# Kernel tuning notes

Hardware: AMD Instinct MI355X
Metric: run time of the kernel (lower is better)

## Reference

```python
import jax, jax.numpy as jnp
import numpy as np

B, S, D = 2, 2048, 1024
H = 16
HD = D // H
SCALE = float(np.sqrt(HD))


def setup_inputs() -> dict:
    key = jax.random.key(0)
    ks = jax.random.split(key, 10)
    def lin(k):
        # xavier_uniform for [out, in] = [D, D]
        bound = float(np.sqrt(6.0 / (D + D)))
        return jax.random.uniform(k, (D, D), jnp.float32, -bound, bound)
    return {
        "hidden_states": jax.random.normal(ks[0], (B, S, D), jnp.float32),
        "attention_mask": jnp.ones((B, S), jnp.float32),
        "Wq": lin(ks[1]), "bq": jnp.zeros((D,), jnp.float32),
        "Wk": lin(ks[2]), "bk": jnp.zeros((D,), jnp.float32),
        "Wv": lin(ks[3]), "bv": jnp.zeros((D,), jnp.float32),
        "Wo": lin(ks[4]), "bo": jnp.zeros((D,), jnp.float32),
    }


def _heads(x):
    # [B,S,D] -> [B,H,S,HD]
    return x.reshape(B, S, H, HD).transpose(0, 2, 1, 3)


def secure_softmax(scores):
    c = jnp.clip(scores, -3.0, 3.0)
    sig = 0.5 + 0.25 * c - 0.01 * c ** 3
    sig = jnp.clip(sig, 0.01, 0.99)
    return sig / (jnp.sum(sig, axis=-1, keepdims=True) + 1e-8)


def reference(hidden_states, attention_mask, Wq, bq, Wk, bk, Wv, bv, Wo, bo):
    q = _heads(hidden_states @ Wq.T + bq)
    k = _heads(hidden_states @ Wk.T + bk)
    v = _heads(hidden_states @ Wv.T + bv)
    # [B,H,S,S]
    scores = jnp.einsum("bhqd,bhkd->bhqk", q, k) / SCALE
    scores = scores + (1.0 - attention_mask[:, None, None, :]) * -10000.0
    probs = secure_softmax(scores)
    ctx = jnp.einsum("bhqk,bhkd->bhqd", probs, v)
    ctx = ctx.transpose(0, 2, 1, 3).reshape(B, S, D)
    return ctx @ Wo.T + bo
```

## Files before the change

### kernel.cpp

```cpp
#include <hip/hip_runtime.h>
#include <stdint.h>

#define B_ 2
#define S_ 2048
#define D_ 1024
#define H_ 16
#define HD_ 64
#define M_ (B_*S_)

typedef __bf16 bf16;
typedef __attribute__((ext_vector_type(8))) __bf16 bf16x8;
typedef __attribute__((ext_vector_type(4))) float f32x4;
typedef __attribute__((ext_vector_type(2))) float f32x2;

__device__ __forceinline__ void gload16(const bf16* g, bf16* l) {
    __builtin_amdgcn_global_load_lds(
        (const __attribute__((address_space(1))) void*)g,
        (__attribute__((address_space(3))) void*)l, 16, 0, 0);
}

__global__ void k_cvt_all(const float* __restrict__ hs,
                          const float* __restrict__ Wq, const float* __restrict__ Wk,
                          const float* __restrict__ Wv, const float* __restrict__ Wo,
                          bf16* __restrict__ hb,
                          bf16* __restrict__ wqb, bf16* __restrict__ wkb,
                          bf16* __restrict__ wvb, bf16* __restrict__ wob) {
    int blk = blockIdx.x;
    const float* s; bf16* d; int base;
    if (blk < 2048) { s = hs; d = hb; base = blk; }
    else {
        int r = blk - 2048; int which = r >> 9; base = r & 511;
        s = (which==0)?Wq:(which==1)?Wk:(which==2)?Wv:Wo;
        d = (which==0)?wqb:(which==1)?wkb:(which==2)?wvb:wob;
    }
    int idx = base*2048 + threadIdx.x*8;
    float4 a = *(const float4*)(s + idx);
    float4 b = *(const float4*)(s + idx + 4);
    bf16 o[8] = {(bf16)a.x,(bf16)a.y,(bf16)a.z,(bf16)a.w,
                 (bf16)b.x,(bf16)b.y,(bf16)b.z,(bf16)b.w};
    *(int4*)(d + idx) = *(const int4*)o;
}

__global__ __launch_bounds__(256) void k_gemm_qkv(
    const bf16* __restrict__ X,
    const bf16* __restrict__ Wq, const bf16* __restrict__ Wk, const bf16* __restrict__ Wv,
    const float* __restrict__ bq, const float* __restrict__ bk, const float* __restrict__ bv,
    bf16* __restrict__ Qo, bf16* __restrict__ Ko, bf16* __restrict__ Vo)
{
    const int z = blockIdx.z;
    const bf16* W = (z==0) ? Wq : (z==1) ? Wk : Wv;
    const float* bias = (z==0) ? bq : (z==1) ? bk : bv;
    const int n0 = blockIdx.x * 128;
    const int m0 = blockIdx.y * 128;
    const int t = threadIdx.x;
    const int w = t >> 6, lane = t & 63, quad = lane >> 4, l15 = lane & 15;
    const int lr = lane >> 3;
    const int lc = (lane & 7) ^ lr;
    const int sx = l15 & 7;
    const int mw = (w >> 1) * 64, nw = (w & 1) * 64;

    __shared__ __align__(16) char smraw[128*136*2];
    bf16* As  = (bf16*)smraw;
    bf16* Bs  = (bf16*)(smraw + 16384);
    bf16* epi = (bf16*)smraw;

    f32x4 acc[4][4];
    #pragma unroll
    for (int i = 0; i < 4; i++)
        #pragma unroll
        for (int j = 0; j < 4; j++)
            acc[i][j] = (f32x4){0.f,0.f,0.f,0.f};

    const bf16* gA = X + (size_t)(m0 + w*8 + lr)*D_ + lc*8;
    const bf16* gB = W + (size_t)(n0 + w*8 + lr)*D_ + lc*8;

    for (int k0 = 0; k0 < D_; k0 += 64) {
        #pragma unroll
        for (int c = 0; c < 4; c++) {
            gload16(gA + (size_t)c*32*D_ + k0, &As[c*2048 + w*512]);
            gload16(gB + (size_t)c*32*D_ + k0, &Bs[c*2048 + w*512]);
        }
        __syncthreads();
        #pragma unroll
        for (int ks = 0; ks < 2; ks++) {
            bf16x8 af[4], bfr[4];
            #pragma unroll
            for (int i = 0; i < 4; i++)
                af[i] = *(const bf16x8*)&As[(mw + i*16 + l15)*64 + (((ks*4+quad)^sx)*8)];
            #pragma unroll
            for (int j = 0; j < 4; j++)
                bfr[j] = *(const bf16x8*)&Bs[(nw + j*16 + l15)*64 + (((ks*4+quad)^sx)*8)];
            #pragma unroll
            for (int i = 0; i < 4; i++)
                #pragma unroll
                for (int j = 0; j < 4; j++)
                    acc[i][j] = __builtin_amdgcn_mfma_f32_16x16x32_bf16(af[i], bfr[j], acc[i][j], 0, 0, 0);
        }
        __syncthreads();
    }

    const float scale = (z == 0) ? 0.125f : 1.0f;
    if (z == 2) {
        #pragma unroll
        for (int j = 0; j < 4; j++) {
            int n = nw + j*16 + l15;
            float bn = bias[n0 + n];
            #pragma unroll
            for (int i = 0; i < 4; i++) {
                int mloc = mw + i*16 + quad*4;
                union { bf16 h4[4]; uint2 u; } pk;
                #pragma unroll
                for (int r = 0; r < 4; r++) pk.h4[r] = (bf16)(acc[i][j][r] + bn);
                *(uint2*)&epi[n*136 + mloc] = pk.u;
            }
        }
    } else {
        #pragma unroll
        for (int j = 0; j < 4; j++) {
            int n = nw + j*16 + l15;
            float bn = bias[n0 + n];
            #pragma unroll
            for (int i = 0; i < 4; i++) {
                int mloc = mw + i*16 + quad*4;
                #pragma unroll
                for (int r = 0; r < 4; r++)
                    epi[(mloc + r)*136 + n] = (bf16)((acc[i][j][r] + bn) * scale);
            }
        }
    }
    __syncthreads();
    if (z == 2) {
        #pragma unroll
        for (int kk = 0; kk < 8; kk++) {
            int c = t + 256*kk;
            int row = c >> 4;
            int mcol = (c & 15) * 8;
            int4 val = *(const int4*)&epi[row*136 + mcol];
            int n = n0 + row; int hh = n >> 6, hd = n & 63;
            int m = m0 + mcol; int bb = m >> 11, s = m & 2047;
            *(int4*)&Vo[((size_t)((bb*H_ + hh)*HD_ + hd))*S_ + s] = val;
        }
    } else {
        bf16* Out = (z == 0) ? Qo : Ko;
        #pragma unroll
        for (int kk = 0; kk < 8; kk++) {
            int c = t + 256*kk;
            int row = c >> 4;
            int ncol = (c & 15) * 8;
            int4 val = *(const int4*)&epi[row*136 + ncol];
            int m = m0 + row; int bb = m >> 11, s = m & 2047;
            int n = n0 + ncol; int hh = n >> 6, hd = n & 63;
            *(int4*)&Out[((size_t)((bb*H_ + hh)*S_ + s))*HD_ + hd] = val;
        }
    }
}

__global__ __launch_bounds__(256) void k_gemm_out(
    const bf16* __restrict__ X, const bf16* __restrict__ W,
    const float* __restrict__ bias, float* __restrict__ Out)
{
    const int n0 = blockIdx.x * 128;
    const int m0 = blockIdx.y * 64;
    const int t = threadIdx.x;
    const int w = t >> 6, lane = t & 63, quad = lane >> 4, l15 = lane & 15;
    const int lr = lane >> 3;
    const int lc = (lane & 7) ^ lr;
    const int sx = l15 & 7;
    const int nw = w * 32;

    __shared__ __align__(16) bf16 As[64*64];
    __shared__ __align__(16) bf16 Bs[128*64];

    f32x4 acc[4][2];
    #pragma unroll
    for (int i = 0; i < 4; i++)
        #pragma unroll
        for (int j = 0; j < 2; j++)
            acc[i][j] = (f32x4){0.f,0.f,0.f,0.f};

    const bf16* gA = X + (size_t)(m0 + w*8 + lr)*D_ + lc*8;
    const bf16* gB = W + (size_t)(n0 + w*8 + lr)*D_ + lc*8;

    for (int k0 = 0; k0 < D_; k0 += 64) {
        #pragma unroll
        for (int c = 0; c < 2; c++)
            gload16(gA + (size_t)c*32*D_ + k0, &As[c*2048 + w*512]);
        #pragma unroll
        for (int c = 0; c < 4; c++)
            gload16(gB + (size_t)c*32*D_ + k0, &Bs[c*2048 + w*512]);
        __syncthreads();
        #pragma unroll
        for (int ks = 0; ks < 2; ks++) {
            bf16x8 af[4], bfr[2];
            #pragma unroll
            for (int i = 0; i < 4; i++)
                af[i] = *(const bf16x8*)&As[(i*16 + l15)*64 + (((ks*4+quad)^sx)*8)];
            #pragma unroll
            for (int j = 0; j < 2; j++)
                bfr[j] = *(const bf16x8*)&Bs[(nw + j*16 + l15)*64 + (((ks*4+quad)^sx)*8)];
            #pragma unroll
            for (int i = 0; i < 4; i++)
                #pragma unroll
                for (int j = 0; j < 2; j++)
                    acc[i][j] = __builtin_amdgcn_mfma_f32_16x16x32_bf16(af[i], bfr[j], acc[i][j], 0, 0, 0);
        }
        __syncthreads();
    }

    #pragma unroll
    for (int j = 0; j < 2; j++) {
        int n = n0 + nw + j*16 + l15;
        float bn = bias[n];
        #pragma unroll
        for (int i = 0; i < 4; i++) {
            int mbase = m0 + i*16 + quad*4;
            #pragma unroll
            for (int r = 0; r < 4; r++)
                Out[(size_t)(mbase + r)*D_ + n] = acc[i][j][r] + bn;
        }
    }
}

__global__ __launch_bounds__(256, 2) void k_attn(
    const bf16* __restrict__ Q, const bf16* __restrict__ K, const bf16* __restrict__ Vt,
    const float* __restrict__ mask, bf16* __restrict__ Ctx)
{
    const int bh = blockIdx.y;
    const int b = bh >> 4, h = bh & 15;
    const int q0 = blockIdx.x * 128;
    const int t = threadIdx.x;
    const int w = t >> 6, lane = t & 63, quad = lane >> 4, l15 = lane & 15;
    const int lr = lane >> 3;
    const int lcV = (lane & 7) ^ lr;
    const int lcK = (lane & 7) ^ ((lr & 3) | ((w & 1) << 2));
    const int sx = l15 & 7;
    const int arow = ((l15 & 12) << 1) | (l15 & 3);

    __shared__ __align__(16) bf16 Ks[2][64*64];
    __shared__ __align__(16) bf16 Vs[2][64*64];

    bf16x8 qf[2][2];
    const bf16* Qbase = Q + ((size_t)bh*S_ + q0 + w*32)*HD_;
    #pragma unroll
    for (int m2 = 0; m2 < 2; m2++)
        #pragma unroll
        for (int ks = 0; ks < 2; ks++)
            qf[m2][ks] = *(const bf16x8*)&Qbase[(size_t)(m2*16 + l15)*HD_ + ks*32 + quad*8];

    f32x4 cacc[2][4];
    #pragma unroll
    for (int i = 0; i < 2; i++)
        #pragma unroll
        for (int j = 0; j < 4; j++)
            cacc[i][j] = (f32x4){0.f,0.f,0.f,0.f};
    f32x2 lacv[2];
    #pragma unroll
    for (int m2 = 0; m2 < 2; m2++) lacv[m2] = (f32x2){0.f,0.f};

    const bf16* KstK = K  + ((size_t)bh*S_  + w*8 + lr)*HD_ + lcK*8;
    const bf16* VstV = Vt + ((size_t)bh*HD_ + w*8 + lr)*S_  + lcV*8;
    const float* mrow = mask + (size_t)b*S_ + quad*8;

    #pragma unroll
    for (int c = 0; c < 2; c++)
        gload16(KstK + (size_t)c*32*HD_, &Ks[0][c*2048 + w*512]);
    #pragma unroll
    for (int c = 0; c < 2; c++)
        gload16(VstV + (size_t)c*32*S_, &Vs[0][c*2048 + w*512]);
    float4 m4[4], m4n[4];
    #pragma unroll
    for (int g = 0; g < 4; g++)
        m4[g] = *(const float4*)&mrow[(g>>1)*32 + (g&1)*4];
    __syncthreads();

    for (int it = 0; it < S_/64; it++) {
        const int cur = it & 1, nxt = cur ^ 1;
        const int k1 = it*64 + 64;
        const bool notlast = (it < S_/64 - 1);

        if (notlast) {
            #pragma unroll
            for (int c = 0; c < 2; c++)
                gload16(KstK + (size_t)(k1 + c*32)*HD_, &Ks[nxt][c*2048 + w*512]);
            #pragma unroll
            for (int c = 0; c < 2; c++)
                gload16(VstV + (size_t)c*32*S_ + k1, &Vs[nxt][c*2048 + w*512]);
            #pragma unroll
            for (int g = 0; g < 4; g++)
                m4n[g] = *(const float4*)&mrow[k1 + (g>>1)*32 + (g&1)*4];
        }

        f32x4 st[4][2];
        #pragma unroll
        for (int g = 0; g < 4; g++) {
            f32x4 sti = (f32x4){m4[g].x, m4[g].y, m4[g].z, m4[g].w} * 10000.f - 10000.f;
            st[g][0] = sti;
            st[g][1] = sti;
        }

        __builtin_amdgcn_s_setprio(1);
        #pragma unroll
        for (int ks = 0; ks < 2; ks++) {
            #pragma unroll
            for (int g = 0; g < 4; g++) {
                const int kk = g >> 1, hf = g & 1;
                bf16x8 af = *(const bf16x8*)&Ks[cur][(arow + hf*4 + kk*32)*64 + (((ks*4+quad)^sx)*8)];
                #pragma unroll
                for (int m2 = 0; m2 < 2; m2++)
                    st[g][m2] = __builtin_amdgcn_mfma_f32_16x16x32_bf16(af, qf[m2][ks], st[g][m2], 0, 0, 0);
            }
        }
        __builtin_amdgcn_s_setprio(0);

        const f32x2 vn3 = {-3.f, -3.f}, vp3 = {3.f, 3.f};
        bf16x8 pa[2][2];
        #pragma unroll
        for (int m2 = 0; m2 < 2; m2++) {
            #pragma unroll
            for (int kk = 0; kk < 2; kk++) {
                union { bf16 h8[8]; bf16x8 v; } pk;
                #pragma unroll
                for (int hf = 0; hf < 2; hf++) {
                    f32x4 sv = st[kk*2 + hf][m2];
                    f32x2 lo = {sv[0], sv[1]};
                    f32x2 hi = {sv[2], sv[3]};
                    lo = __builtin_elementwise_min(__builtin_elementwise_max(lo, vn3), vp3);
                    hi = __builtin_elementwise_min(__builtin_elementwise_max(hi, vn3), vp3);
                    f32x2 tlo = lo * lo * (-0.01f) + 0.25f;
                    f32x2 thi = hi * hi * (-0.01f) + 0.25f;
                    f32x2 slo = lo * tlo + 0.5f;
                    f32x2 shi = hi * thi + 0.5f;
                    lacv[m2] += slo;
                    lacv[m2] += shi;
                    pk.h8[hf*4+0] = (bf16)slo.x; pk.h8[hf*4+1] = (bf16)slo.y;
                    pk.h8[hf*4+2] = (bf16)shi.x; pk.h8[hf*4+3] = (bf16)shi.y;
                }
                pa[m2][kk] = pk.v;
            }
        }

        #pragma unroll
        for (int kk = 0; kk < 2; kk++) {
            bf16x8 vf[4];
            #pragma unroll
            for (int nt = 0; nt < 4; nt++)
                vf[nt] = *(const bf16x8*)&Vs[cur][(nt*16 + l15)*64 + (((kk*4+quad)^sx)*8)];
            __builtin_amdgcn_s_setprio(1);
            #pragma unroll
            for (int m2 = 0; m2 < 2; m2++)
                #pragma unroll
                for (int nt = 0; nt < 4; nt++)
                    cacc[m2][nt] = __builtin_amdgcn_mfma_f32_16x16x32_bf16(pa[m2][kk], vf[nt], cacc[m2][nt], 0, 0, 0);
            __builtin_amdgcn_s_setprio(0);
        }

        __syncthreads();

        #pragma unroll
        for (int g = 0; g < 4; g++) m4[g] = m4n[g];
    }

    float s[2];
    #pragma unroll
    for (int m2 = 0; m2 < 2; m2++) {
        float v = lacv[m2].x + lacv[m2].y;
        v += __shfl_xor(v, 16);
        v += __shfl_xor(v, 32);
        s[m2] = v;
    }

    #pragma unroll
    for (int m2 = 0; m2 < 2; m2++) {
        #pragma unroll
        for (int r = 0; r < 4; r++) {
            float rs = __shfl(s[m2], quad*4 + r);
            float rinv = 1.0f / (rs + 1e-8f);
            size_t row = (size_t)(b*S_ + q0 + w*32 + m2*16 + quad*4 + r);
            #pragma unroll
            for (int nt = 0; nt < 4; nt++)
                Ctx[row*D_ + h*HD_ + nt*16 + l15] = (bf16)(cacc[m2][nt][r] * rinv);
        }
    }
}

extern "C" void kernel_launch(void* const* d_in, const int* in_sizes, int n_in,
                              void* d_out, int out_size, void* d_ws, size_t ws_size,
                              hipStream_t stream) {
    const float* hs   = (const float*)d_in[0];
    const float* mask = (const float*)d_in[1];
    const float* Wq   = (const float*)d_in[2];
    const float* bq   = (const float*)d_in[3];
    const float* Wk   = (const float*)d_in[4];
    const float* bk   = (const float*)d_in[5];
    const float* Wv   = (const float*)d_in[6];
    const float* bv   = (const float*)d_in[7];
    const float* Wo   = (const float*)d_in[8];
    const float* bo   = (const float*)d_in[9];
    float* out = (float*)d_out;

    char* ws = (char*)d_ws;
    const size_t MB = 1024*1024;
    bf16* hb   = (bf16*)(ws);
    bf16* wqb  = (bf16*)(ws + 8*MB);
    bf16* wkb  = (bf16*)(ws + 10*MB);
    bf16* wvb  = (bf16*)(ws + 12*MB);
    bf16* wob  = (bf16*)(ws + 14*MB);
    bf16* qb   = (bf16*)(ws + 16*MB);
    bf16* kb   = (bf16*)(ws + 24*MB);
    bf16* vtb  = (bf16*)(ws + 32*MB);
    bf16* ctxb = (bf16*)(ws + 40*MB);

    k_cvt_all<<<2048 + 4*512, 256, 0, stream>>>(hs, Wq, Wk, Wv, Wo, hb, wqb, wkb, wvb, wob);

    k_gemm_qkv<<<dim3(D_/128, M_/128, 3), 256, 0, stream>>>(
        hb, wqb, wkb, wvb, bq, bk, bv, qb, kb, vtb);

    k_attn<<<dim3(S_/128, B_*H_), 256, 0, stream>>>(qb, kb, vtb, mask, ctxb);

    k_gemm_out<<<dim3(D_/128, M_/64), 256, 0, stream>>>(ctxb, wob, bo, out);
}
```

Baseline: 199.8 us.

## Split attention block work across eight waves of sixteen query rows

```diff
diff --git a/kernel.cpp b/kernel.cpp
--- a/kernel.cpp
+++ b/kernel.cpp
@@ -221,7 +221,7 @@
     }
 }
 
-__global__ __launch_bounds__(256, 2) void k_attn(
+__global__ __launch_bounds__(512, 4) void k_attn(
     const bf16* __restrict__ Q, const bf16* __restrict__ K, const bf16* __restrict__ Vt,
     const float* __restrict__ mask, bf16* __restrict__ Ctx)
 {
@@ -239,34 +239,24 @@
     __shared__ __align__(16) bf16 Ks[2][64*64];
     __shared__ __align__(16) bf16 Vs[2][64*64];
 
-    bf16x8 qf[2][2];
-    const bf16* Qbase = Q + ((size_t)bh*S_ + q0 + w*32)*HD_;
-    #pragma unroll
-    for (int m2 = 0; m2 < 2; m2++)
-        #pragma unroll
-        for (int ks = 0; ks < 2; ks++)
-            qf[m2][ks] = *(const bf16x8*)&Qbase[(size_t)(m2*16 + l15)*HD_ + ks*32 + quad*8];
-
-    f32x4 cacc[2][4];
-    #pragma unroll
-    for (int i = 0; i < 2; i++)
-        #pragma unroll
-        for (int j = 0; j < 4; j++)
-            cacc[i][j] = (f32x4){0.f,0.f,0.f,0.f};
-    f32x2 lacv[2];
-    #pragma unroll
-    for (int m2 = 0; m2 < 2; m2++) lacv[m2] = (f32x2){0.f,0.f};
+    bf16x8 qf[2];
+    const bf16* Qbase = Q + ((size_t)bh*S_ + q0 + w*16)*HD_;
+    #pragma unroll
+    for (int ks = 0; ks < 2; ks++)
+        qf[ks] = *(const bf16x8*)&Qbase[(size_t)l15*HD_ + ks*32 + quad*8];
+
+    f32x4 cacc[4];
+    #pragma unroll
+    for (int j = 0; j < 4; j++)
+        cacc[j] = (f32x4){0.f,0.f,0.f,0.f};
+    f32x2 lacv = (f32x2){0.f,0.f};
 
     const bf16* KstK = K  + ((size_t)bh*S_  + w*8 + lr)*HD_ + lcK*8;
     const bf16* VstV = Vt + ((size_t)bh*HD_ + w*8 + lr)*S_  + lcV*8;
     const float* mrow = mask + (size_t)b*S_ + quad*8;
 
-    #pragma unroll
-    for (int c = 0; c < 2; c++)
-        gload16(KstK + (size_t)c*32*HD_, &Ks[0][c*2048 + w*512]);
-    #pragma unroll
-    for (int c = 0; c < 2; c++)
-        gload16(VstV + (size_t)c*32*S_, &Vs[0][c*2048 + w*512]);
+    gload16(KstK, &Ks[0][w*512]);
+    gload16(VstV, &Vs[0][w*512]);
     float4 m4[4], m4n[4];
     #pragma unroll
     for (int g = 0; g < 4; g++)
@@ -279,24 +269,17 @@
         const bool notlast = (it < S_/64 - 1);
 
         if (notlast) {
-            #pragma unroll
-            for (int c = 0; c < 2; c++)
-                gload16(KstK + (size_t)(k1 + c*32)*HD_, &Ks[nxt][c*2048 + w*512]);
-            #pragma unroll
-            for (int c = 0; c < 2; c++)
-                gload16(VstV + (size_t)c*32*S_ + k1, &Vs[nxt][c*2048 + w*512]);
+            gload16(KstK + (size_t)k1*HD_, &Ks[nxt][w*512]);
+            gload16(VstV + k1,             &Vs[nxt][w*512]);
             #pragma unroll
             for (int g = 0; g < 4; g++)
                 m4n[g] = *(const float4*)&mrow[k1 + (g>>1)*32 + (g&1)*4];
         }
 
-        f32x4 st[4][2];
-        #pragma unroll
-        for (int g = 0; g < 4; g++) {
-            f32x4 sti = (f32x4){m4[g].x, m4[g].y, m4[g].z, m4[g].w} * 10000.f - 10000.f;
-            st[g][0] = sti;
-            st[g][1] = sti;
-        }
+        f32x4 st[4];
+        #pragma unroll
+        for (int g = 0; g < 4; g++)
+            st[g] = (f32x4){m4[g].x, m4[g].y, m4[g].z, m4[g].w} * 10000.f - 10000.f;
 
         __builtin_amdgcn_s_setprio(1);
         #pragma unroll
@@ -305,38 +288,33 @@
             for (int g = 0; g < 4; g++) {
                 const int kk = g >> 1, hf = g & 1;
                 bf16x8 af = *(const bf16x8*)&Ks[cur][(arow + hf*4 + kk*32)*64 + (((ks*4+quad)^sx)*8)];
-                #pragma unroll
-                for (int m2 = 0; m2 < 2; m2++)
-                    st[g][m2] = __builtin_amdgcn_mfma_f32_16x16x32_bf16(af, qf[m2][ks], st[g][m2], 0, 0, 0);
+                st[g] = __builtin_amdgcn_mfma_f32_16x16x32_bf16(af, qf[ks], st[g], 0, 0, 0);
             }
         }
         __builtin_amdgcn_s_setprio(0);
 
         const f32x2 vn3 = {-3.f, -3.f}, vp3 = {3.f, 3.f};
-        bf16x8 pa[2][2];
-        #pragma unroll
-        for (int m2 = 0; m2 < 2; m2++) {
-            #pragma unroll
-            for (int kk = 0; kk < 2; kk++) {
-                union { bf16 h8[8]; bf16x8 v; } pk;
-                #pragma unroll
-                for (int hf = 0; hf < 2; hf++) {
-                    f32x4 sv = st[kk*2 + hf][m2];
-                    f32x2 lo = {sv[0], sv[1]};
-                    f32x2 hi = {sv[2], sv[3]};
-                    lo = __builtin_elementwise_min(__builtin_elementwise_max(lo, vn3), vp3);
-                    hi = __builtin_elementwise_min(__builtin_elementwise_max(hi, vn3), vp3);
-                    f32x2 tlo = lo * lo * (-0.01f) + 0.25f;
-                    f32x2 thi = hi * hi * (-0.01f) + 0.25f;
-                    f32x2 slo = lo * tlo + 0.5f;
-                    f32x2 shi = hi * thi + 0.5f;
-                    lacv[m2] += slo;
-                    lacv[m2] += shi;
-                    pk.h8[hf*4+0] = (bf16)slo.x; pk.h8[hf*4+1] = (bf16)slo.y;
-                    pk.h8[hf*4+2] = (bf16)shi.x; pk.h8[hf*4+3] = (bf16)shi.y;
-                }
-                pa[m2][kk] = pk.v;
+        bf16x8 pa[2];
+        #pragma unroll
+        for (int kk = 0; kk < 2; kk++) {
+            union { bf16 h8[8]; bf16x8 v; } pk;
+            #pragma unroll
+            for (int hf = 0; hf < 2; hf++) {
+                f32x4 sv = st[kk*2 + hf];
+                f32x2 lo = {sv[0], sv[1]};
+                f32x2 hi = {sv[2], sv[3]};
+                lo = __builtin_elementwise_min(__builtin_elementwise_max(lo, vn3), vp3);
+                hi = __builtin_elementwise_min(__builtin_elementwise_max(hi, vn3), vp3);
+                f32x2 tlo = lo * lo * (-0.01f) + 0.25f;
+                f32x2 thi = hi * hi * (-0.01f) + 0.25f;
+                f32x2 slo = lo * tlo + 0.5f;
+                f32x2 shi = hi * thi + 0.5f;
+                lacv += slo;
+                lacv += shi;
+                pk.h8[hf*4+0] = (bf16)slo.x; pk.h8[hf*4+1] = (bf16)slo.y;
+                pk.h8[hf*4+2] = (bf16)shi.x; pk.h8[hf*4+3] = (bf16)shi.y;
             }
+            pa[kk] = pk.v;
         }
 
         #pragma unroll
@@ -347,10 +325,8 @@
                 vf[nt] = *(const bf16x8*)&Vs[cur][(nt*16 + l15)*64 + (((kk*4+quad)^sx)*8)];
             __builtin_amdgcn_s_setprio(1);
             #pragma unroll
-            for (int m2 = 0; m2 < 2; m2++)
-                #pragma unroll
-                for (int nt = 0; nt < 4; nt++)
-                    cacc[m2][nt] = __builtin_amdgcn_mfma_f32_16x16x32_bf16(pa[m2][kk], vf[nt], cacc[m2][nt], 0, 0, 0);
+            for (int nt = 0; nt < 4; nt++)
+                cacc[nt] = __builtin_amdgcn_mfma_f32_16x16x32_bf16(pa[kk], vf[nt], cacc[nt], 0, 0, 0);
             __builtin_amdgcn_s_setprio(0);
         }
 
@@ -360,26 +336,22 @@
         for (int g = 0; g < 4; g++) m4[g] = m4n[g];
     }
 
-    float s[2];
-    #pragma unroll
-    for (int m2 = 0; m2 < 2; m2++) {
-        float v = lacv[m2].x + lacv[m2].y;
+    float s;
+    {
+        float v = lacv.x + lacv.y;
         v += __shfl_xor(v, 16);
         v += __shfl_xor(v, 32);
-        s[m2] = v;
-    }
-
-    #pragma unroll
-    for (int m2 = 0; m2 < 2; m2++) {
-        #pragma unroll
-        for (int r = 0; r < 4; r++) {
-            float rs = __shfl(s[m2], quad*4 + r);
-            float rinv = 1.0f / (rs + 1e-8f);
-            size_t row = (size_t)(b*S_ + q0 + w*32 + m2*16 + quad*4 + r);
-            #pragma unroll
-            for (int nt = 0; nt < 4; nt++)
-                Ctx[row*D_ + h*HD_ + nt*16 + l15] = (bf16)(cacc[m2][nt][r] * rinv);
-        }
+        s = v;
+    }
+
+    #pragma unroll
+    for (int r = 0; r < 4; r++) {
+        float rs = __shfl(s, quad*4 + r);
+        float rinv = 1.0f / (rs + 1e-8f);
+        size_t row = (size_t)(b*S_ + q0 + w*16 + quad*4 + r);
+        #pragma unroll
+        for (int nt = 0; nt < 4; nt++)
+            Ctx[row*D_ + h*HD_ + nt*16 + l15] = (bf16)(cacc[nt][r] * rinv);
     }
 }
 
@@ -415,7 +387,7 @@
     k_gemm_qkv<<<dim3(D_/128, M_/128, 3), 256, 0, stream>>>(
         hb, wqb, wkb, wvb, bq, bk, bv, qb, kb, vtb);
 
-    k_attn<<<dim3(S_/128, B_*H_), 256, 0, stream>>>(qb, kb, vtb, mask, ctxb);
+    k_attn<<<dim3(S_/128, B_*H_), 512, 0, stream>>>(qb, kb, vtb, mask, ctxb);
 
     k_gemm_out<<<dim3(D_/128, M_/64), 256, 0, stream>>>(ctxb, wob, bo, out);
 }
```

Result: no change. 202.1 us (+1.2%).

## Deepen K/V prefetch to two tiles ahead and stage mask in LDS

Applied to the files above, without the earlier changes.

```diff
diff --git a/kernel.cpp b/kernel.cpp
--- a/kernel.cpp
+++ b/kernel.cpp
@@ -236,8 +236,9 @@
     const int sx = l15 & 7;
     const int arow = ((l15 & 12) << 1) | (l15 & 3);
 
-    __shared__ __align__(16) bf16 Ks[2][64*64];
-    __shared__ __align__(16) bf16 Vs[2][64*64];
+    __shared__ __align__(16) bf16 Ks[4][64*64];
+    __shared__ __align__(16) bf16 Vs[4][64*64];
+    __shared__ __align__(16) float Ms[S_];
 
     bf16x8 qf[2][2];
     const bf16* Qbase = Q + ((size_t)bh*S_ + q0 + w*32)*HD_;
@@ -259,41 +260,43 @@
 
     const bf16* KstK = K  + ((size_t)bh*S_  + w*8 + lr)*HD_ + lcK*8;
     const bf16* VstV = Vt + ((size_t)bh*HD_ + w*8 + lr)*S_  + lcV*8;
-    const float* mrow = mask + (size_t)b*S_ + quad*8;
-
-    #pragma unroll
-    for (int c = 0; c < 2; c++)
-        gload16(KstK + (size_t)c*32*HD_, &Ks[0][c*2048 + w*512]);
-    #pragma unroll
-    for (int c = 0; c < 2; c++)
-        gload16(VstV + (size_t)c*32*S_, &Vs[0][c*2048 + w*512]);
-    float4 m4[4], m4n[4];
-    #pragma unroll
-    for (int g = 0; g < 4; g++)
-        m4[g] = *(const float4*)&mrow[(g>>1)*32 + (g&1)*4];
-    __syncthreads();
-
-    for (int it = 0; it < S_/64; it++) {
-        const int cur = it & 1, nxt = cur ^ 1;
-        const int k1 = it*64 + 64;
-        const bool notlast = (it < S_/64 - 1);
-
-        if (notlast) {
-            #pragma unroll
-            for (int c = 0; c < 2; c++)
-                gload16(KstK + (size_t)(k1 + c*32)*HD_, &Ks[nxt][c*2048 + w*512]);
-            #pragma unroll
-            for (int c = 0; c < 2; c++)
-                gload16(VstV + (size_t)c*32*S_ + k1, &Vs[nxt][c*2048 + w*512]);
-            #pragma unroll
-            for (int g = 0; g < 4; g++)
-                m4n[g] = *(const float4*)&mrow[k1 + (g>>1)*32 + (g&1)*4];
+
+    {
+        const float* mg = mask + (size_t)b*S_ + t*8;
+        float4 a0 = *(const float4*)mg;
+        float4 a1 = *(const float4*)(mg + 4);
+        *(float4*)&Ms[t*8]     = a0;
+        *(float4*)&Ms[t*8 + 4] = a1;
+    }
+    #pragma unroll
+    for (int pt = 0; pt < 2; pt++)
+        #pragma unroll
+        for (int c = 0; c < 2; c++) {
+            gload16(KstK + (size_t)(pt*64 + c*32)*HD_, &Ks[pt][c*2048 + w*512]);
+            gload16(VstV + (size_t)c*32*S_ + pt*64,    &Vs[pt][c*2048 + w*512]);
+        }
+    asm volatile("s_waitcnt vmcnt(4) lgkmcnt(0)\n\ts_barrier" ::: "memory");
+
+    const int NT = S_/64;
+    for (int it = 0; it < NT; it++) {
+        const int cur = it & 3;
+        const int k0 = it*64;
+
+        if (it < NT-2) {
+            const int pb = (it + 2) & 3;
+            const int kp = k0 + 128;
+            #pragma unroll
+            for (int c = 0; c < 2; c++) {
+                gload16(KstK + (size_t)(kp + c*32)*HD_, &Ks[pb][c*2048 + w*512]);
+                gload16(VstV + (size_t)c*32*S_ + kp,    &Vs[pb][c*2048 + w*512]);
+            }
         }
 
         f32x4 st[4][2];
         #pragma unroll
         for (int g = 0; g < 4; g++) {
-            f32x4 sti = (f32x4){m4[g].x, m4[g].y, m4[g].z, m4[g].w} * 10000.f - 10000.f;
+            float4 m4 = *(const float4*)&Ms[k0 + quad*8 + (g>>1)*32 + (g&1)*4];
+            f32x4 sti = (f32x4){m4.x, m4.y, m4.z, m4.w} * 10000.f - 10000.f;
             st[g][0] = sti;
             st[g][1] = sti;
         }
@@ -354,10 +357,10 @@
             __builtin_amdgcn_s_setprio(0);
         }
 
-        __syncthreads();
-
-        #pragma unroll
-        for (int g = 0; g < 4; g++) m4[g] = m4n[g];
+        if (it < NT-2)
+            asm volatile("s_waitcnt vmcnt(4)\n\ts_barrier" ::: "memory");
+        else
+            asm volatile("s_waitcnt vmcnt(0)\n\ts_barrier" ::: "memory");
     }
 
     float s[2];
```

Result: no change. 200.9 us (+0.6%).

## Split attention over key halves, fuse QKV per head, add combine kernel

Applied to the files above, without the earlier changes.

```diff
diff --git a/kernel.cpp b/kernel.cpp
--- a/kernel.cpp
+++ b/kernel.cpp
@@ -47,110 +47,122 @@
     const float* __restrict__ bq, const float* __restrict__ bk, const float* __restrict__ bv,
     bf16* __restrict__ Qo, bf16* __restrict__ Ko, bf16* __restrict__ Vo)
 {
-    const int z = blockIdx.z;
-    const bf16* W = (z==0) ? Wq : (z==1) ? Wk : Wv;
-    const float* bias = (z==0) ? bq : (z==1) ? bk : bv;
-    const int n0 = blockIdx.x * 128;
+    const int hh = blockIdx.x;
+    const int n0 = hh * 64;
     const int m0 = blockIdx.y * 128;
     const int t = threadIdx.x;
     const int w = t >> 6, lane = t & 63, quad = lane >> 4, l15 = lane & 15;
     const int lr = lane >> 3;
     const int lc = (lane & 7) ^ lr;
     const int sx = l15 & 7;
-    const int mw = (w >> 1) * 64, nw = (w & 1) * 64;
-
-    __shared__ __align__(16) char smraw[128*136*2];
+    const int mw = (w >> 1) * 64, nw = (w & 1) * 32;
+
+    __shared__ __align__(16) char smraw[40960];
     bf16* As  = (bf16*)smraw;
-    bf16* Bs  = (bf16*)(smraw + 16384);
+    bf16* Bsf = (bf16*)(smraw + 16384);
     bf16* epi = (bf16*)smraw;
 
-    f32x4 acc[4][4];
-    #pragma unroll
-    for (int i = 0; i < 4; i++)
-        #pragma unroll
-        for (int j = 0; j < 4; j++)
-            acc[i][j] = (f32x4){0.f,0.f,0.f,0.f};
+    f32x4 acc[3][4][2];
+    #pragma unroll
+    for (int z = 0; z < 3; z++)
+        #pragma unroll
+        for (int i = 0; i < 4; i++)
+            #pragma unroll
+            for (int j = 0; j < 2; j++)
+                acc[z][i][j] = (f32x4){0.f,0.f,0.f,0.f};
 
     const bf16* gA = X + (size_t)(m0 + w*8 + lr)*D_ + lc*8;
-    const bf16* gB = W + (size_t)(n0 + w*8 + lr)*D_ + lc*8;
+    const bf16* Wz[3] = {Wq, Wk, Wv};
+    const bf16* gB[6];
+    #pragma unroll
+    for (int cc = 0; cc < 6; cc++) {
+        const int z = cc >> 1;
+        const int rowz = (cc & 1)*32 + w*8 + lr;
+        gB[cc] = Wz[z] + (size_t)(n0 + rowz)*D_ + lc*8;
+    }
 
     for (int k0 = 0; k0 < D_; k0 += 64) {
         #pragma unroll
-        for (int c = 0; c < 4; c++) {
+        for (int c = 0; c < 4; c++)
             gload16(gA + (size_t)c*32*D_ + k0, &As[c*2048 + w*512]);
-            gload16(gB + (size_t)c*32*D_ + k0, &Bs[c*2048 + w*512]);
-        }
+        #pragma unroll
+        for (int cc = 0; cc < 6; cc++)
+            gload16(gB[cc] + k0, &Bsf[cc*2048 + w*512]);
         __syncthreads();
         #pragma unroll
         for (int ks = 0; ks < 2; ks++) {
-            bf16x8 af[4], bfr[4];
+            bf16x8 af[4], bfr[3][2];
             #pragma unroll
             for (int i = 0; i < 4; i++)
                 af[i] = *(const bf16x8*)&As[(mw + i*16 + l15)*64 + (((ks*4+quad)^sx)*8)];
             #pragma unroll
-            for (int j = 0; j < 4; j++)
-                bfr[j] = *(const bf16x8*)&Bs[(nw + j*16 + l15)*64 + (((ks*4+quad)^sx)*8)];
-            #pragma unroll
-            for (int i = 0; i < 4; i++)
-                #pragma unroll
-                for (int j = 0; j < 4; j++)
-                    acc[i][j] = __builtin_amdgcn_mfma_f32_16x16x32_bf16(af[i], bfr[j], acc[i][j], 0, 0, 0);
-        }
-        __syncthreads();
-    }
-
-    const float scale = (z == 0) ? 0.125f : 1.0f;
-    if (z == 2) {
-        #pragma unroll
-        for (int j = 0; j < 4; j++) {
+            for (int z = 0; z < 3; z++)
+                #pragma unroll
+                for (int j = 0; j < 2; j++)
+                    bfr[z][j] = *(const bf16x8*)&Bsf[z*4096 + (nw + j*16 + l15)*64 + (((ks*4+quad)^sx)*8)];
+            #pragma unroll
+            for (int z = 0; z < 3; z++)
+                #pragma unroll
+                for (int i = 0; i < 4; i++)
+                    #pragma unroll
+                    for (int j = 0; j < 2; j++)
+                        acc[z][i][j] = __builtin_amdgcn_mfma_f32_16x16x32_bf16(af[i], bfr[z][j], acc[z][i][j], 0, 0, 0);
+        }
+        __syncthreads();
+    }
+
+    #pragma unroll
+    for (int z = 0; z < 2; z++) {
+        const float scale = z ? 1.0f : 0.125f;
+        const float* bias = z ? bk : bq;
+        bf16* Out = z ? Ko : Qo;
+        #pragma unroll
+        for (int j = 0; j < 2; j++) {
             int n = nw + j*16 + l15;
             float bn = bias[n0 + n];
+            #pragma unroll
+            for (int i = 0; i < 4; i++) {
+                int mloc = mw + i*16 + quad*4;
+                #pragma unroll
+                for (int r = 0; r < 4; r++)
+                    epi[(mloc + r)*72 + n] = (bf16)((acc[z][i][j][r] + bn) * scale);
+            }
+        }
+        __syncthreads();
+        #pragma unroll
+        for (int p = 0; p < 4; p++) {
+            int c = t + 256*p;
+            int row = c >> 3;
+            int ncol = (c & 7) * 8;
+            int4 val = *(const int4*)&epi[row*72 + ncol];
+            int m = m0 + row; int bb = m >> 11, s = m & 2047;
+            *(int4*)&Out[((size_t)((bb*H_ + hh)*S_ + s))*HD_ + ncol] = val;
+        }
+        __syncthreads();
+    }
+    {
+        #pragma unroll
+        for (int j = 0; j < 2; j++) {
+            int n = nw + j*16 + l15;
+            float bn = bv[n0 + n];
             #pragma unroll
             for (int i = 0; i < 4; i++) {
                 int mloc = mw + i*16 + quad*4;
                 union { bf16 h4[4]; uint2 u; } pk;
                 #pragma unroll
-                for (int r = 0; r < 4; r++) pk.h4[r] = (bf16)(acc[i][j][r] + bn);
+                for (int r = 0; r < 4; r++) pk.h4[r] = (bf16)(acc[2][i][j][r] + bn);
                 *(uint2*)&epi[n*136 + mloc] = pk.u;
             }
         }
-    } else {
-        #pragma unroll
-        for (int j = 0; j < 4; j++) {
-            int n = nw + j*16 + l15;
-            float bn = bias[n0 + n];
-            #pragma unroll
-            for (int i = 0; i < 4; i++) {
-                int mloc = mw + i*16 + quad*4;
-                #pragma unroll
-                for (int r = 0; r < 4; r++)
-                    epi[(mloc + r)*136 + n] = (bf16)((acc[i][j][r] + bn) * scale);
-            }
-        }
-    }
-    __syncthreads();
-    if (z == 2) {
-        #pragma unroll
-        for (int kk = 0; kk < 8; kk++) {
-            int c = t + 256*kk;
+        __syncthreads();
+        #pragma unroll
+        for (int p = 0; p < 4; p++) {
+            int c = t + 256*p;
             int row = c >> 4;
             int mcol = (c & 15) * 8;
             int4 val = *(const int4*)&epi[row*136 + mcol];
-            int n = n0 + row; int hh = n >> 6, hd = n & 63;
             int m = m0 + mcol; int bb = m >> 11, s = m & 2047;
-            *(int4*)&Vo[((size_t)((bb*H_ + hh)*HD_ + hd))*S_ + s] = val;
-        }
-    } else {
-        bf16* Out = (z == 0) ? Qo : Ko;
-        #pragma unroll
-        for (int kk = 0; kk < 8; kk++) {
-            int c = t + 256*kk;
-            int row = c >> 4;
-            int ncol = (c & 15) * 8;
-            int4 val = *(const int4*)&epi[row*136 + ncol];
-            int m = m0 + row; int bb = m >> 11, s = m & 2047;
-            int n = n0 + ncol; int hh = n >> 6, hd = n & 63;
-            *(int4*)&Out[((size_t)((bb*H_ + hh)*S_ + s))*HD_ + hd] = val;
+            *(int4*)&Vo[((size_t)((bb*H_ + hh)*HD_ + row))*S_ + s] = val;
         }
     }
 }
@@ -221,13 +233,16 @@
     }
 }
 
-__global__ __launch_bounds__(256, 2) void k_attn(
+__global__ __launch_bounds__(256, 4) void k_attn(
     const bf16* __restrict__ Q, const bf16* __restrict__ K, const bf16* __restrict__ Vt,
-    const float* __restrict__ mask, bf16* __restrict__ Ctx)
+    const float* __restrict__ mask,
+    float* __restrict__ Cp, float* __restrict__ Sp)
 {
     const int bh = blockIdx.y;
     const int b = bh >> 4, h = bh & 15;
     const int q0 = blockIdx.x * 128;
+    const int z = blockIdx.z;
+    const int kbase = z * (S_/2);
     const int t = threadIdx.x;
     const int w = t >> 6, lane = t & 63, quad = lane >> 4, l15 = lane & 15;
     const int lr = lane >> 3;
@@ -257,34 +272,33 @@
     #pragma unroll
     for (int m2 = 0; m2 < 2; m2++) lacv[m2] = (f32x2){0.f,0.f};
 
-    const bf16* KstK = K  + ((size_t)bh*S_  + w*8 + lr)*HD_ + lcK*8;
-    const bf16* VstV = Vt + ((size_t)bh*HD_ + w*8 + lr)*S_  + lcV*8;
-    const float* mrow = mask + (size_t)b*S_ + quad*8;
-
-    #pragma unroll
-    for (int c = 0; c < 2; c++)
-        gload16(KstK + (size_t)c*32*HD_, &Ks[0][c*2048 + w*512]);
-    #pragma unroll
-    for (int c = 0; c < 2; c++)
-        gload16(VstV + (size_t)c*32*S_, &Vs[0][c*2048 + w*512]);
+    const bf16* KstK = K  + ((size_t)bh*S_ + kbase + w*8 + lr)*HD_ + lcK*8;
+    const bf16* VstV = Vt + ((size_t)bh*HD_ + w*8 + lr)*S_ + kbase + lcV*8;
+    const float* mrow = mask + (size_t)b*S_ + kbase + quad*8;
+
+    #pragma unroll
+    for (int c = 0; c < 2; c++) {
+        gload16(KstK + (size_t)(c*32)*HD_, &Ks[0][c*2048 + w*512]);
+        gload16(VstV + (size_t)c*32*S_,    &Vs[0][c*2048 + w*512]);
+    }
     float4 m4[4], m4n[4];
     #pragma unroll
     for (int g = 0; g < 4; g++)
         m4[g] = *(const float4*)&mrow[(g>>1)*32 + (g&1)*4];
-    __syncthreads();
-
-    for (int it = 0; it < S_/64; it++) {
+    asm volatile("s_waitcnt vmcnt(0)\n\ts_barrier" ::: "memory");
+
+    const int NT = S_/128;
+    for (int it = 0; it < NT; it++) {
         const int cur = it & 1, nxt = cur ^ 1;
         const int k1 = it*64 + 64;
-        const bool notlast = (it < S_/64 - 1);
+        const bool notlast = (it < NT - 1);
 
         if (notlast) {
             #pragma unroll
-            for (int c = 0; c < 2; c++)
+            for (int c = 0; c < 2; c++) {
                 gload16(KstK + (size_t)(k1 + c*32)*HD_, &Ks[nxt][c*2048 + w*512]);
-            #pragma unroll
-            for (int c = 0; c < 2; c++)
-                gload16(VstV + (size_t)c*32*S_ + k1, &Vs[nxt][c*2048 + w*512]);
+                gload16(VstV + (size_t)c*32*S_ + k1,    &Vs[nxt][c*2048 + w*512]);
+            }
             #pragma unroll
             for (int g = 0; g < 4; g++)
                 m4n[g] = *(const float4*)&mrow[k1 + (g>>1)*32 + (g&1)*4];
@@ -312,7 +326,6 @@
         }
         __builtin_amdgcn_s_setprio(0);
 
-        const f32x2 vn3 = {-3.f, -3.f}, vp3 = {3.f, 3.f};
         bf16x8 pa[2][2];
         #pragma unroll
         for (int m2 = 0; m2 < 2; m2++) {
@@ -322,10 +335,11 @@
                 #pragma unroll
                 for (int hf = 0; hf < 2; hf++) {
                     f32x4 sv = st[kk*2 + hf][m2];
-                    f32x2 lo = {sv[0], sv[1]};
-                    f32x2 hi = {sv[2], sv[3]};
-                    lo = __builtin_elementwise_min(__builtin_elementwise_max(lo, vn3), vp3);
-                    hi = __builtin_elementwise_min(__builtin_elementwise_max(hi, vn3), vp3);
+                    f32x2 lo, hi;
+                    lo.x = __builtin_amdgcn_fmed3f(sv[0], -3.f, 3.f);
+                    lo.y = __builtin_amdgcn_fmed3f(sv[1], -3.f, 3.f);
+                    hi.x = __builtin_amdgcn_fmed3f(sv[2], -3.f, 3.f);
+                    hi.y = __builtin_amdgcn_fmed3f(sv[3], -3.f, 3.f);
                     f32x2 tlo = lo * lo * (-0.01f) + 0.25f;
                     f32x2 thi = hi * hi * (-0.01f) + 0.25f;
                     f32x2 slo = lo * tlo + 0.5f;
@@ -354,33 +368,57 @@
             __builtin_amdgcn_s_setprio(0);
         }
 
-        __syncthreads();
+        asm volatile("s_waitcnt vmcnt(0)\n\ts_barrier" ::: "memory");
 
         #pragma unroll
         for (int g = 0; g < 4; g++) m4[g] = m4n[g];
     }
 
-    float s[2];
     #pragma unroll
     for (int m2 = 0; m2 < 2; m2++) {
         float v = lacv[m2].x + lacv[m2].y;
         v += __shfl_xor(v, 16);
         v += __shfl_xor(v, 32);
-        s[m2] = v;
-    }
-
+        if (quad == 0)
+            Sp[((size_t)z*B_*H_ + bh)*S_ + q0 + w*32 + m2*16 + l15] = v;
+    }
+
+    float* Cpz = Cp + (size_t)z*M_*D_;
     #pragma unroll
     for (int m2 = 0; m2 < 2; m2++) {
         #pragma unroll
         for (int r = 0; r < 4; r++) {
-            float rs = __shfl(s[m2], quad*4 + r);
-            float rinv = 1.0f / (rs + 1e-8f);
             size_t row = (size_t)(b*S_ + q0 + w*32 + m2*16 + quad*4 + r);
             #pragma unroll
             for (int nt = 0; nt < 4; nt++)
-                Ctx[row*D_ + h*HD_ + nt*16 + l15] = (bf16)(cacc[m2][nt][r] * rinv);
-        }
-    }
+                Cpz[row*D_ + h*HD_ + nt*16 + l15] = cacc[m2][nt][r];
+        }
+    }
+}
+
+__global__ __launch_bounds__(256) void k_combine(
+    const float* __restrict__ Cp, const float* __restrict__ Sp,
+    bf16* __restrict__ Ctx)
+{
+    int idx = (blockIdx.x*256 + threadIdx.x) * 8;
+    int r  = idx >> 10;
+    int dc = idx & 1023;
+    int hh = dc >> 6;
+    int bb = r >> 11, q = r & 2047;
+    float s0 = Sp[(size_t)(bb*H_ + hh)*S_ + q];
+    float s1 = Sp[(size_t)(B_*H_ + bb*H_ + hh)*S_ + q];
+    float rinv = 1.0f / (s0 + s1 + 1e-8f);
+    const float* c0 = Cp + (size_t)r*D_ + dc;
+    const float* c1 = c0 + (size_t)M_*D_;
+    float4 a0 = *(const float4*)c0;
+    float4 a1 = *(const float4*)(c0 + 4);
+    float4 b0 = *(const float4*)c1;
+    float4 b1 = *(const float4*)(c1 + 4);
+    bf16 o[8] = {(bf16)((a0.x+b0.x)*rinv), (bf16)((a0.y+b0.y)*rinv),
+                 (bf16)((a0.z+b0.z)*rinv), (bf16)((a0.w+b0.w)*rinv),
+                 (bf16)((a1.x+b1.x)*rinv), (bf16)((a1.y+b1.y)*rinv),
+                 (bf16)((a1.z+b1.z)*rinv), (bf16)((a1.w+b1.w)*rinv)};
+    *(int4*)(Ctx + idx) = *(const int4*)o;
 }
 
 extern "C" void kernel_launch(void* const* d_in, const int* in_sizes, int n_in,
@@ -409,13 +447,17 @@
     bf16* kb   = (bf16*)(ws + 24*MB);
     bf16* vtb  = (bf16*)(ws + 32*MB);
     bf16* ctxb = (bf16*)(ws + 40*MB);
+    float* Cp  = (float*)(ws + 48*MB);
+    float* Sp  = (float*)(ws + 80*MB);
 
     k_cvt_all<<<2048 + 4*512, 256, 0, stream>>>(hs, Wq, Wk, Wv, Wo, hb, wqb, wkb, wvb, wob);
 
-    k_gemm_qkv<<<dim3(D_/128, M_/128, 3), 256, 0, stream>>>(
+    k_gemm_qkv<<<dim3(H_, M_/128), 256, 0, stream>>>(
         hb, wqb, wkb, wvb, bq, bk, bv, qb, kb, vtb);
 
-    k_attn<<<dim3(S_/128, B_*H_), 256, 0, stream>>>(qb, kb, vtb, mask, ctxb);
+    k_attn<<<dim3(S_/128, B_*H_, 2), 256, 0, stream>>>(qb, kb, vtb, mask, Cp, Sp);
+
+    k_combine<<<M_*D_/(256*8), 256, 0, stream>>>(Cp, Sp, ctxb);
 
     k_gemm_out<<<dim3(D_/128, M_/64), 256, 0, stream>>>(ctxb, wob, bo, out);
 }
```

Result: no change. 198.9 us (-0.4%).
